# Performance work log

Hardware: AMD Instinct MI355X
Metric: run time of the kernel (lower is better)

The kernel has to match this reference:

```python
import jax, jax.numpy as jnp
import numpy as np

NUM_HEADS = 8
BN_EPS = 1e-5
NORM_EPS = 1e-12


def setup_inputs() -> dict:
    key = jax.random.key(0)
    ks = jax.random.split(key, 5)
    b, c, h, w = 4, 256, 128, 128
    cr = c // 16  # reduced channels in the gating branch
    return {
        "x": jax.random.normal(ks[0], (b, c, h, w), dtype=jnp.float32),
        "temperature": jnp.ones((NUM_HEADS, 1, 1), dtype=jnp.float32),
        "w1": jax.random.normal(ks[1], (cr, c), dtype=jnp.float32) * 0.05,
        "b1": jnp.zeros((cr,), dtype=jnp.float32),
        "bn_gamma": jnp.ones((cr,), dtype=jnp.float32),
        "bn_beta": jnp.zeros((cr,), dtype=jnp.float32),
        "bn_mean": jnp.zeros((cr,), dtype=jnp.float32),
        "bn_var": jnp.ones((cr,), dtype=jnp.float32),
        "w2": jax.random.normal(ks[2], (c, cr), dtype=jnp.float32) * 0.1,
        "b2": jnp.zeros((c,), dtype=jnp.float32),
        "proj_w": jax.random.normal(ks[3], (c, 2 * c), dtype=jnp.float32) * 0.05,
    }


def _complex_softmax(a, axis=-1):
    return jax.lax.complex(jax.nn.softmax(a.real, axis=axis),
                           jax.nn.softmax(a.imag, axis=axis))


def reference(x, temperature, w1, b1, bn_gamma, bn_beta, bn_mean, bn_var, w2, b2, proj_w):
    b, c, h, w = x.shape
    hd = NUM_HEADS
    xf = jnp.fft.fft2(x)

    # q = k = v = fft2(x), reshaped to (b, head, c/head, h*w)
    qkv = xf.reshape(b, hd, c // hd, h * w)
    # F.normalize over last dim: divide by L2 norm (complex norm = sqrt(sum |.|^2))
    nrm = jnp.sqrt(jnp.sum(qkv.real**2 + qkv.imag**2, axis=-1, keepdims=True))
    qn = qkv / jnp.maximum(nrm, NORM_EPS)

    # channel attention: (b, head, c', c'), contract over spatial freq dim
    attn = jnp.einsum('bhcn,bhdn->bhcd', qn, qn) * temperature.astype(xf.dtype)
    attn = _complex_softmax(attn, axis=-1)

    out = jnp.einsum('bhcd,bhdn->bhcn', attn, qkv)
    # torch.fft.ifft2 on a 4D tensor acts over the last two dims (c', h*w)
    out_f = jnp.abs(jnp.fft.ifft2(out)).reshape(b, c, h, w)

    # gating branch: conv1x1 -> BN(inference) -> ReLU -> conv1x1 -> sigmoid on real(fft2(x))
    y = jnp.einsum('bchw,oc->bohw', xf.real, w1) + b1[:, None, None]
    y = (y - bn_mean[:, None, None]) / jnp.sqrt(bn_var[:, None, None] + BN_EPS)
    y = y * bn_gamma[:, None, None] + bn_beta[:, None, None]
    y = jax.nn.relu(y)
    y = jnp.einsum('bchw,oc->bohw', y, w2) + b2[:, None, None]
    gate = jax.nn.sigmoid(y)

    out_f_l = jnp.abs(jnp.fft.ifft2(gate * xf))

    cat = jnp.concatenate([out_f, out_f_l], axis=1)  # (b, 2c, h, w)
    return jnp.einsum('bchw,oc->bohw', cat, proj_w)
```

## Files before the change

### kernel.cpp

```cpp
#include <hip/hip_runtime.h>
#include <math.h>

#define NFFT 16384
static constexpr size_t NP = 16777216;

typedef short bf16x8 __attribute__((ext_vector_type(8)));
typedef __fp16 f16x8 __attribute__((ext_vector_type(8)));
typedef float f32x4  __attribute__((ext_vector_type(4)));
typedef __fp16 h16x2 __attribute__((ext_vector_type(2)));

union FU  { bf16x8 v; unsigned u[4]; };
union FU16{ f16x8  v; unsigned u[4]; };

__device__ __forceinline__ void sincos_rev(float rv, float& sn, float& cs){
    sn = __builtin_amdgcn_sinf(rv);
    cs = __builtin_amdgcn_cosf(rv);
}
__device__ __forceinline__ int rev7(int v){ return (int)(__brev((unsigned)v) >> 25); }

__device__ __forceinline__ unsigned f2bf(float f){
    unsigned u = __float_as_uint(f);
    return (u + 0x7FFFu + ((u >> 16) & 1u)) >> 16;
}
__device__ __forceinline__ float bf2f(unsigned h){ return __uint_as_float(h << 16); }
__device__ __forceinline__ unsigned packsplit(float v){
    unsigned h = f2bf(v);
    float r = v - bf2f(h);
    unsigned l = f2bf(r);
    return (h << 16) | l;
}

union HU2 { h16x2 h; unsigned u; };
__device__ __forceinline__ unsigned packh(float a, float b){
    HU2 z; z.h = __builtin_amdgcn_cvt_pkrtz(a, b); return z.u;
}
__device__ __forceinline__ void unpackh(unsigned u, float& a, float& b){
    HU2 z; z.u = u; a = (float)z.h.x; b = (float)z.h.y;
}

struct TwF { float cw[6], sw[6], sg[6], c6, s6; };
__device__ __forceinline__ void make_twf(TwF& t){
    const int l = threadIdx.x & 63;
    #pragma unroll
    for (int lg = 0; lg < 6; ++lg){
        int m = 1 << lg;
        bool up = (l & m) != 0;
        int e = (l & (m-1)) * (64 >> lg);
        float sn, cs; sincos_rev((float)e * 0.0078125f, sn, cs);
        t.cw[lg] = up ? cs : 1.f;
        t.sw[lg] = up ? -sn : 0.f;
        t.sg[lg] = up ? -1.f : 1.f;
    }
    sincos_rev((float)l * 0.0078125f, t.s6, t.c6);
}
struct TwI { float cw[6], sw[6], c6, s6; };
__device__ __forceinline__ void make_twi(TwI& t){
    const int l = threadIdx.x & 63;
    #pragma unroll
    for (int lg = 0; lg < 6; ++lg){
        int m = 1 << lg;
        bool up = (l & m) != 0;
        int e = (l & (m-1)) * (64 >> lg);
        float sn, cs; sincos_rev((float)e * 0.0078125f, sn, cs);
        t.cw[lg] = up ? -cs : cs;
        t.sw[lg] = up ? -sn : sn;
    }
    sincos_rev((float)l * 0.0078125f, t.s6, t.c6);
}

__device__ __forceinline__ void dif128t(const TwF& t, float& r0, float& i0, float& r1, float& i1){
    {
        float ar = r0 + r1, ai = i0 + i1;
        float br = r0 - r1, bi = i0 - i1;
        r0 = ar; i0 = ai;
        r1 =  br*t.c6 + bi*t.s6;
        i1 = -br*t.s6 + bi*t.c6;
    }
    #pragma unroll
    for (int lg = 5; lg >= 0; --lg){
        int m = 1 << lg;
        float cw = t.cw[lg], sw = t.sw[lg], sg = t.sg[lg];
        float pr = __shfl_xor(r0, m, 64), pi = __shfl_xor(i0, m, 64);
        float tr = fmaf(sg, r0, pr), ti = fmaf(sg, i0, pi);
        r0 = tr*cw - ti*sw;
        i0 = tr*sw + ti*cw;
        pr = __shfl_xor(r1, m, 64); pi = __shfl_xor(i1, m, 64);
        tr = fmaf(sg, r1, pr); ti = fmaf(sg, i1, pi);
        r1 = tr*cw - ti*sw;
        i1 = tr*sw + ti*cw;
    }
}

__device__ __forceinline__ void dit128t(const TwI& t, float& r0, float& i0, float& r1, float& i1){
    const int l = threadIdx.x & 63;
    #pragma unroll
    for (int lg = 0; lg <= 5; ++lg){
        int m = 1 << lg;
        bool up = (l & m) != 0;
        float cw = t.cw[lg], sw = t.sw[lg];
        float pr = __shfl_xor(r0, m, 64), pi = __shfl_xor(i0, m, 64);
        float vr = up ? r0 : pr, vi = up ? i0 : pi;
        float ar = up ? pr : r0, ai = up ? pi : i0;
        r0 = fmaf(vr, cw, fmaf(vi, -sw, ar));
        i0 = fmaf(vr, sw, fmaf(vi,  cw, ai));
        pr = __shfl_xor(r1, m, 64); pi = __shfl_xor(i1, m, 64);
        vr = up ? r1 : pr; vi = up ? i1 : pi;
        ar = up ? pr : r1; ai = up ? pi : i1;
        r1 = fmaf(vr, cw, fmaf(vi, -sw, ar));
        i1 = fmaf(vr, sw, fmaf(vi,  cw, ai));
    }
    {
        float wr = r1*t.c6 - i1*t.s6, wi = r1*t.s6 + i1*t.c6;
        float ar = r0 + wr, ai = i0 + wi;
        r1 = r0 - wr; i1 = i0 - wi;
        r0 = ar; i0 = ai;
    }
}

__global__ __launch_bounds__(1024, 8) void k_fft2_fwd(const float* __restrict__ x,
                                                   unsigned* __restrict__ spR, unsigned* __restrict__ spI,
                                                   float* __restrict__ norm2){
    __shared__ unsigned sp[128*129];
    __shared__ float red[16];
    int lane = threadIdx.x & 63, wave = threadIdx.x >> 6;
    int img = blockIdx.x;
    TwF tw; make_twf(tw);
    const float* base = x + (size_t)img * NFFT;
    #pragma unroll 2
    for (int it = 0; it < 8; ++it){
        int h = (wave << 3) + it;
        float a0 = base[h*128 + lane], b0 = 0.f;
        float a1 = base[h*128 + lane + 64], b1 = 0.f;
        dif128t(tw, a0, b0, a1, b1);
        sp[lane*129 + h]      = packh(a0, b0);
        sp[(lane+64)*129 + h] = packh(a1, b1);
    }
    __syncthreads();
    float acc = 0.f;
    #pragma unroll 2
    for (int it = 0; it < 8; ++it){
        int j = (wave << 3) + it;
        float a0, b0, a1, b1;
        unpackh(sp[j*129 + lane],      a0, b0);
        unpackh(sp[j*129 + lane + 64], a1, b1);
        dif128t(tw, a0, b0, a1, b1);
        acc += a0*a0 + b0*b0 + a1*a1 + b1*b1;
        float t0 = __shfl_xor(a0, 1, 64), u0 = __shfl_xor(b0, 1, 64);
        float t1 = __shfl_xor(a1, 1, 64), u1 = __shfl_xor(b1, 1, 64);
        size_t m = (size_t)img*8192 + (size_t)j*64;
        int k = lane >> 1;
        if (!(lane & 1)){
            spR[m + k]      = packh(a0, t0);
            spR[m + 32 + k] = packh(a1, t1);
        } else {
            spI[m + k]      = packh(u0, b0);
            spI[m + 32 + k] = packh(u1, b1);
        }
    }
    #pragma unroll
    for (int m = 32; m >= 1; m >>= 1) acc += __shfl_xor(acc, m, 64);
    if (lane == 0) red[wave] = acc;
    __syncthreads();
    if (threadIdx.x == 0){
        float s = 0.f;
        #pragma unroll
        for (int i = 0; i < 16; ++i) s += red[i];
        norm2[img] = s;
    }
}

__global__ __launch_bounds__(256) void k_gram(const unsigned* __restrict__ spR, const unsigned* __restrict__ spI,
                                              float* __restrict__ Gpart){
    __shared__ unsigned lds[2*32*132];
    int t = threadIdx.x, lane = t & 63, wave = t >> 6;
    int bh = blockIdx.x >> 5;
    int ks = blockIdx.x & 31;
    size_t cbase2 = (size_t)bh * 32 * 8192;
    int k0blk = ks << 9;

    int sc = t >> 3, tk = t & 7;

    f32x4 aRe[2][2], aIm[2][2];
    #pragma unroll
    for (int i = 0; i < 2; ++i)
        #pragma unroll
        for (int j = 0; j < 2; ++j){ aRe[i][j] = (f32x4){0,0,0,0}; aIm[i][j] = (f32x4){0,0,0,0}; }

    for (int tile = 0; tile < 2; ++tile){
        int kb = k0blk + (tile << 8);
        __syncthreads();
        {
            const unsigned* pr  = spR + cbase2 + (size_t)sc*8192 + (kb >> 1) + tk*16;
            const unsigned* pi_ = spI + cbase2 + (size_t)sc*8192 + (kb >> 1) + tk*16;
            unsigned* dr = &lds[sc*132 + tk*16];
            unsigned* di = &lds[32*132 + sc*132 + tk*16];
            #pragma unroll
            for (int j = 0; j < 4; ++j){
                *(uint4*)(dr + 4*j) = *(const uint4*)(pr + 4*j);
                *(uint4*)(di + 4*j) = *(const uint4*)(pi_ + 4*j);
            }
        }
        __syncthreads();
        #pragma unroll
        for (int ss = 0; ss < 2; ++ss){
            int s = wave + (ss << 2);
            int kbase = (s << 4) + ((lane >> 4) << 2);
            FU16 fr0, fr1, fi0, fi1, fn0, fn1;
            *(uint4*)fr0.u = *(const uint4*)&lds[ (lane & 15)*132 + kbase ];
            *(uint4*)fr1.u = *(const uint4*)&lds[ ((lane & 15) + 16)*132 + kbase ];
            *(uint4*)fi0.u = *(const uint4*)&lds[ 32*132 + (lane & 15)*132 + kbase ];
            *(uint4*)fi1.u = *(const uint4*)&lds[ 32*132 + ((lane & 15) + 16)*132 + kbase ];
            #pragma unroll
            for (int p = 0; p < 4; ++p){ fn0.u[p] = fi0.u[p] ^ 0x80008000u; fn1.u[p] = fi1.u[p] ^ 0x80008000u; }
            aRe[0][0] = __builtin_amdgcn_mfma_f32_16x16x32_f16(fr0.v, fr0.v, aRe[0][0], 0, 0, 0);
            aRe[0][0] = __builtin_amdgcn_mfma_f32_16x16x32_f16(fn0.v, fi0.v, aRe[0][0], 0, 0, 0);
            aRe[0][1] = __builtin_amdgcn_mfma_f32_16x16x32_f16(fr0.v, fr1.v, aRe[0][1], 0, 0, 0);
            aRe[0][1] = __builtin_amdgcn_mfma_f32_16x16x32_f16(fn0.v, fi1.v, aRe[0][1], 0, 0, 0);
            aRe[1][0] = __builtin_amdgcn_mfma_f32_16x16x32_f16(fr1.v, fr0.v, aRe[1][0], 0, 0, 0);
            aRe[1][0] = __builtin_amdgcn_mfma_f32_16x16x32_f16(fn1.v, fi0.v, aRe[1][0], 0, 0, 0);
            aRe[1][1] = __builtin_amdgcn_mfma_f32_16x16x32_f16(fr1.v, fr1.v, aRe[1][1], 0, 0, 0);
            aRe[1][1] = __builtin_amdgcn_mfma_f32_16x16x32_f16(fn1.v, fi1.v, aRe[1][1], 0, 0, 0);
            aIm[0][0] = __builtin_amdgcn_mfma_f32_16x16x32_f16(fr0.v, fi0.v, aIm[0][0], 0, 0, 0);
            aIm[0][0] = __builtin_amdgcn_mfma_f32_16x16x32_f16(fi0.v, fr0.v, aIm[0][0], 0, 0, 0);
            aIm[0][1] = __builtin_amdgcn_mfma_f32_16x16x32_f16(fr0.v, fi1.v, aIm[0][1], 0, 0, 0);
            aIm[0][1] = __builtin_amdgcn_mfma_f32_16x16x32_f16(fi0.v, fr1.v, aIm[0][1], 0, 0, 0);
            aIm[1][0] = __builtin_amdgcn_mfma_f32_16x16x32_f16(fr1.v, fi0.v, aIm[1][0], 0, 0, 0);
            aIm[1][0] = __builtin_amdgcn_mfma_f32_16x16x32_f16(fi1.v, fr0.v, aIm[1][0], 0, 0, 0);
            aIm[1][1] = __builtin_amdgcn_mfma_f32_16x16x32_f16(fr1.v, fi1.v, aIm[1][1], 0, 0, 0);
            aIm[1][1] = __builtin_amdgcn_mfma_f32_16x16x32_f16(fi1.v, fr1.v, aIm[1][1], 0, 0, 0);
        }
    }
    __syncthreads();
    float* rbuf = (float*)lds;
    int dcol = lane & 15, rrow = lane >> 4;
    #pragma unroll
    for (int i = 0; i < 2; ++i)
        #pragma unroll
        for (int j = 0; j < 2; ++j)
            #pragma unroll
            for (int r = 0; r < 4; ++r){
                int c = (i << 4) + (rrow << 2) + r;
                int d = (j << 4) + dcol;
                rbuf[wave*2048 + ((c << 5) + d)*2    ] = aRe[i][j][r];
                rbuf[wave*2048 + ((c << 5) + d)*2 + 1] = aIm[i][j][r];
            }
    __syncthreads();
    float* gp = Gpart + (size_t)blockIdx.x * 2048;
    for (int idx = t; idx < 2048; idx += 256)
        gp[idx] = rbuf[idx] + rbuf[2048 + idx] + rbuf[4096 + idx] + rbuf[6144 + idx];
}

__global__ __launch_bounds__(256) void k_gram_red(const float* __restrict__ Gpart, float* __restrict__ G){
    int bh = blockIdx.x >> 3;
    int q  = ((blockIdx.x & 7) << 8) + threadIdx.x;
    const float* gp = Gpart + (size_t)bh * 32 * 2048 + q;
    float s = 0.f;
    #pragma unroll 8
    for (int p = 0; p < 32; ++p) s += gp[(size_t)p * 2048];
    G[(size_t)bh * 2048 + q] = s;
}

__global__ __launch_bounds__(256) void k_attn(const float* __restrict__ G, const float* __restrict__ norm2,
                                              const float* __restrict__ temp, float* __restrict__ attn2){
    __shared__ float ar[32*33], ai[32*33];
    int bh = blockIdx.x, h = bh & 7, t = threadIdx.x;
    if (t < 32){
        float tv = temp[h];
        float nc = fmaxf(sqrtf(norm2[(bh<<5) + t]), 1e-12f);
        const float* gr = G + (size_t)bh*2048 + t*64;
        float mr = -1e30f, mi = -1e30f;
        for (int d = 0; d < 32; ++d){
            float nd = fmaxf(sqrtf(norm2[(bh<<5) + d]), 1e-12f);
            float s = tv / (nc * nd);
            float vr = gr[d*2] * s, vi = gr[d*2+1] * s;
            ar[t*33+d] = vr; ai[t*33+d] = vi;
            mr = fmaxf(mr, vr); mi = fmaxf(mi, vi);
        }
        float sr = 0.f, si = 0.f;
        for (int d = 0; d < 32; ++d){
            float er = __expf(ar[t*33+d] - mr), ei = __expf(ai[t*33+d] - mi);
            ar[t*33+d] = er; ai[t*33+d] = ei; sr += er; si += ei;
        }
        sr = 1.f/sr; si = 1.f/si;
        for (int d = 0; d < 32; ++d){ ar[t*33+d] *= sr; ai[t*33+d] *= si; }
    }
    __syncthreads();
    const float S = 1.f / 524288.f;
    for (int q = t; q < 1024; q += 256){
        int e = q >> 5, d = q & 31;
        float sr = 0.f, si = 0.f;
        for (int c = 0; c < 32; ++c){
            float sn, cs; sincos_rev((float)((e*c) & 31) * 0.03125f, sn, cs);
            float xr = ar[c*33+d], xi = ai[c*33+d];
            sr += cs*xr - sn*xi;
            si += cs*xi + sn*xr;
        }
        attn2[(size_t)bh*2048 + q*2]     = sr * S;
        attn2[(size_t)bh*2048 + q*2 + 1] = si * S;
    }
}

__global__ __launch_bounds__(256) void k_mix(const unsigned* __restrict__ spR, const unsigned* __restrict__ spI,
                                             const float* __restrict__ attn2,
                                             unsigned* __restrict__ om){
    __shared__ unsigned lds[2*32*36];
    __shared__ float a2s[2048];
    int t = threadIdx.x, lane = t & 63, wave = t >> 6;
    int quad = lane >> 4, l15 = lane & 15;
    int bh = blockIdx.x >> 5;
    int n0 = (blockIdx.x & 31) << 9;
    size_t cbase2 = (size_t)bh * 32 * 8192;
    {
        const float4* s4 = (const float4*)(attn2 + (size_t)bh*2048);
        float4* d4 = (float4*)a2s;
        d4[t] = s4[t]; d4[t + 256] = s4[t + 256];
    }
    __syncthreads();
    FU16 Ar[2], Ai[2];
    #pragma unroll
    for (int et = 0; et < 2; ++et){
        int e = (et << 4) + l15;
        #pragma unroll
        for (int p = 0; p < 4; ++p){
            int d0 = (quad << 3) + (p << 1);
            Ar[et].u[p] = packh(a2s[(e*32 + d0)*2],     a2s[(e*32 + d0 + 1)*2]);
            Ai[et].u[p] = packh(a2s[(e*32 + d0)*2 + 1], a2s[(e*32 + d0 + 1)*2 + 1]);
        }
    }
    int sd = t >> 3, sc4 = (t & 7) << 2;
    for (int tile = 0; tile < 8; ++tile){
        int nb = n0 + (tile << 6);
        __syncthreads();
        {
            size_t g2 = cbase2 + (size_t)sd*8192 + (nb >> 1) + sc4;
            *(uint4*)&lds[sd*36 + sc4]         = *(const uint4*)&spR[g2];
            *(uint4*)&lds[32*36 + sd*36 + sc4] = *(const uint4*)&spI[g2];
        }
        __syncthreads();
        int colb = (wave << 4) + l15;
        int cb2 = colb >> 1; bool codd = colb & 1;
        FU16 Xr, Xi, Xn;
        #pragma unroll
        for (int p = 0; p < 4; ++p){
            int d0 = (quad << 3) + (p << 1);
            unsigned e0 = lds[d0*36 + cb2], e1 = lds[(d0+1)*36 + cb2];
            Xr.u[p] = codd ? ((e0 >> 16) | (e1 & 0xFFFF0000u)) : ((e0 & 0xFFFFu) | (e1 << 16));
            e0 = lds[32*36 + d0*36 + cb2]; e1 = lds[32*36 + (d0+1)*36 + cb2];
            Xi.u[p] = codd ? ((e0 >> 16) | (e1 & 0xFFFF0000u)) : ((e0 & 0xFFFFu) | (e1 << 16));
            Xn.u[p] = Xi.u[p] ^ 0x80008000u;
        }
        #pragma unroll
        for (int et = 0; et < 2; ++et){
            f32x4 ar = (f32x4){0,0,0,0}, ai = (f32x4){0,0,0,0};
            ar = __builtin_amdgcn_mfma_f32_16x16x32_f16(Ar[et].v, Xr.v, ar, 0, 0, 0);
            ar = __builtin_amdgcn_mfma_f32_16x16x32_f16(Ai[et].v, Xn.v, ar, 0, 0, 0);
            ai = __builtin_amdgcn_mfma_f32_16x16x32_f16(Ar[et].v, Xi.v, ai, 0, 0, 0);
            ai = __builtin_amdgcn_mfma_f32_16x16x32_f16(Ai[et].v, Xr.v, ai, 0, 0, 0);
            #pragma unroll
            for (int r = 0; r < 4; ++r){
                int e = (et << 4) + (quad << 2) + r;
                om[cbase2*2 + (size_t)e*NFFT + nb + colb] = packh(ar[r], ai[r]);
            }
        }
    }
}

__global__ __launch_bounds__(1024, 8) void k_ifft_n(unsigned* io){
    __shared__ unsigned sp[128*129];
    int lane = threadIdx.x & 63, wave = threadIdx.x >> 6;
    size_t rb = (size_t)blockIdx.x * NFFT;
    TwI tw; make_twi(tw);
    #pragma unroll 2
    for (int it = 0; it < 8; ++it){
        int jw = (wave << 3) + it;
        size_t base = rb + ((size_t)jw << 7);
        float a0, b0, a1, b1;
        unpackh(io[base + lane], a0, b0);
        unpackh(io[base + lane + 64], a1, b1);
        dit128t(tw, a0, b0, a1, b1);
        int kw = rev7(jw);
        float sn, cs;
        sincos_rev((float)(lane * kw) * 6.103515625e-05f, sn, cs);
        float r = a0*cs - b0*sn, i2 = a0*sn + b0*cs;
        sp[lane*129 + jw] = packh(r, i2);
        sincos_rev((float)((lane + 64) * kw) * 6.103515625e-05f, sn, cs);
        r = a1*cs - b1*sn; i2 = a1*sn + b1*cs;
        sp[(lane+64)*129 + jw] = packh(r, i2);
    }
    __syncthreads();
    unsigned av[8][2];
    #pragma unroll 2
    for (int it = 0; it < 8; ++it){
        int pw = (wave << 3) + it;
        float a0, b0, a1, b1;
        unpackh(sp[pw*129 + lane],      a0, b0);
        unpackh(sp[pw*129 + lane + 64], a1, b1);
        dit128t(tw, a0, b0, a1, b1);
        av[it][0] = packsplit(sqrtf(a0*a0 + b0*b0));
        av[it][1] = packsplit(sqrtf(a1*a1 + b1*b1));
    }
    __syncthreads();
    #pragma unroll 2
    for (int it = 0; it < 8; ++it){
        int pw = (wave << 3) + it;
        sp[lane*129 + pw] = av[it][0];
        sp[(lane+64)*129 + pw] = av[it][1];
    }
    __syncthreads();
    int row = threadIdx.x >> 3, cb = (threadIdx.x & 7) << 4;
    size_t ob = rb + ((size_t)row << 7) + cb;
    const unsigned* s = &sp[row*129 + cb];
    #pragma unroll
    for (int q = 0; q < 4; ++q)
        *(uint4*)(io + ob + (q << 2)) = make_uint4(s[q*4], s[q*4+1], s[q*4+2], s[q*4+3]);
}

__global__ __launch_bounds__(256) void k_gate(unsigned* spR, unsigned* spI,
                                              const float* __restrict__ w1, const float* __restrict__ b1,
                                              const float* __restrict__ bg, const float* __restrict__ bb_,
                                              const float* __restrict__ bm, const float* __restrict__ bv,
                                              const float* __restrict__ w2, const float* __restrict__ b2){
    __shared__ float w1T[256*17];
    __shared__ float w2s[256*16];
    __shared__ float yred[256*17];
    int t = threadIdx.x, g = t >> 6, col = t & 63;
    #pragma unroll
    for (int i = 0; i < 16; ++i) w1T[t*17 + i] = w1[i*256 + t];
    {
        const float4* s4 = (const float4*)w2; float4* d4 = (float4*)w2s;
        #pragma unroll
        for (int i = 0; i < 4; ++i) d4[i*256 + t] = s4[i*256 + t];
    }
    __syncthreads();
    int b = blockIdx.x >> 8;
    int n = ((blockIdx.x & 255) << 6) + col;
    int odd = n & 1;
    size_t base2 = (((size_t)b << 8) << 13) + (n >> 1);
    float y[16];
    #pragma unroll
    for (int r = 0; r < 16; ++r) y[r] = 0.f;
    for (int c = g << 6; c < (g << 6) + 64; ++c){
        float lo, hi; unpackh(spR[base2 + ((size_t)c << 13)], lo, hi);
        float xr = odd ? hi : lo;
        #pragma unroll
        for (int r = 0; r < 16; ++r) y[r] += w1T[c*17 + r] * xr;
    }
    #pragma unroll
    for (int r = 0; r < 16; ++r) yred[t*17 + r] = y[r];
    __syncthreads();
    #pragma unroll
    for (int r = 0; r < 16; ++r){
        float v = yred[col*17 + r] + yred[(col+64)*17 + r]
                + yred[(col+128)*17 + r] + yred[(col+192)*17 + r] + b1[r];
        v = (v - bm[r]) * rsqrtf(bv[r] + 1e-5f) * bg[r] + bb_[r];
        y[r] = fmaxf(v, 0.f);
    }
    for (int o = g << 6; o < (g << 6) + 64; ++o){
        float s = b2[o];
        #pragma unroll
        for (int r = 0; r < 16; ++r) s += w2s[o*16 + r] * y[r];
        float gg = 1.f / (1.f + __expf(-s)) * 6.103515625e-05f;
        float ggN = __shfl_xor(gg, 1, 64);
        size_t mi = base2 + ((size_t)o << 13);
        if (!odd){
            float lo, hi; unpackh(spR[mi], lo, hi);
            spR[mi] = packh(gg*lo, ggN*hi);
        } else {
            float lo, hi; unpackh(spI[mi], lo, hi);
            spI[mi] = packh(ggN*lo, gg*hi);
        }
    }
}

__global__ __launch_bounds__(1024, 8) void k_ifft2_gate(const unsigned* __restrict__ spR,
                                                        const unsigned* __restrict__ spI,
                                                        unsigned* __restrict__ outp){
    __shared__ unsigned sp[128*129];
    int lane = threadIdx.x & 63, wave = threadIdx.x >> 6;
    size_t ib = (size_t)blockIdx.x * NFFT;
    TwI tw; make_twi(tw);
    #pragma unroll 2
    for (int it = 0; it < 8; ++it){
        int jw = (wave << 3) + it;
        size_t m = (ib + ((size_t)jw << 7)) >> 1;
        int k = lane >> 1; bool od = lane & 1;
        float lo, hi, a0, b0, a1, b1;
        unpackh(spR[m + k], lo, hi);      a0 = od ? hi : lo;
        unpackh(spI[m + k], lo, hi);      b0 = od ? hi : lo;
        unpackh(spR[m + 32 + k], lo, hi); a1 = od ? hi : lo;
        unpackh(spI[m + 32 + k], lo, hi); b1 = od ? hi : lo;
        dit128t(tw, a0, b0, a1, b1);
        sp[lane*129 + jw]      = packh(a0, b0);
        sp[(lane+64)*129 + jw] = packh(a1, b1);
    }
    __syncthreads();
    #pragma unroll 2
    for (int it = 0; it < 8; ++it){
        int ph = (wave << 3) + it;
        float a0, b0, a1, b1;
        unpackh(sp[ph*129 + lane],      a0, b0);
        unpackh(sp[ph*129 + lane + 64], a1, b1);
        dit128t(tw, a0, b0, a1, b1);
        size_t o = ib + ((size_t)ph << 7);
        outp[o + lane]      = packsplit(sqrtf(a0*a0 + b0*b0));
        outp[o + lane + 64] = packsplit(sqrtf(a1*a1 + b1*b1));
    }
}

__global__ __launch_bounds__(256) void k_pw_cvt(const float* __restrict__ pw, unsigned* __restrict__ pwp){
    int i = (blockIdx.x << 10) + (threadIdx.x << 2);
    float4 v = *(const float4*)(pw + i);
    uint4 o;
    o.x = packsplit(v.x); o.y = packsplit(v.y); o.z = packsplit(v.z); o.w = packsplit(v.w);
    *(uint4*)(pwp + i) = o;
}

__global__ __launch_bounds__(256) void k_proj(const unsigned* __restrict__ cat0, const unsigned* __restrict__ cat1,
                                              const unsigned* __restrict__ pwp, float* __restrict__ out){
    __shared__ unsigned As[128*33];
    __shared__ unsigned Bs[32*129];
    int t = threadIdx.x, lane = t & 63, wave = t >> 6;
    int quad = lane >> 4, l15 = lane & 15;
    int b  = blockIdx.x >> 8;
    int mo = (blockIdx.x >> 7) & 1;
    int nt = blockIdx.x & 127;
    int n0 = nt << 7;
    int wr = (wave >> 1) << 6;
    int wc = (wave & 1) << 6;

    f32x4 acc[4][4];
    #pragma unroll
    for (int i = 0; i < 4; ++i)
        #pragma unroll
        for (int j = 0; j < 4; ++j) acc[i][j] = (f32x4){0.f,0.f,0.f,0.f};

    int ao = t >> 1, ak = (t & 1) << 4;
    int bk = t >> 5, bn = t & 31;

    for (int ks = 0; ks < 16; ++ks){
        int k0 = ks << 5;
        __syncthreads();
        {
            const unsigned* ap = pwp + (size_t)((mo << 7) + ao)*512 + k0 + ak;
            #pragma unroll
            for (int i = 0; i < 16; ++i) As[ao*33 + ak + i] = ap[i];
        }
        {
            #pragma unroll
            for (int p = 0; p < 4; ++p){
                int q = k0 + (p << 3) + bk;
                const unsigned* srow = (q < 256) ? (cat0 + (size_t)((b<<8) + q) * NFFT)
                                                 : (cat1 + (size_t)((b<<8) + (q-256)) * NFFT);
                #pragma unroll
                for (int i = 0; i < 4; ++i){
                    int n = bn + (i << 5);
                    Bs[((p<<3) + bk)*129 + n] = srow[n0 + n];
                }
            }
        }
        __syncthreads();
        FU Ah[4], Al[4], Bh[4], Bl[4];
        #pragma unroll
        for (int mi = 0; mi < 4; ++mi){
            const unsigned* ap = &As[(wr + (mi << 4) + l15)*33 + (quad << 3)];
            #pragma unroll
            for (int p = 0; p < 4; ++p){
                unsigned e0 = ap[2*p], e1 = ap[2*p+1];
                Ah[mi].u[p] = (e0 >> 16) | (e1 & 0xFFFF0000u);
                Al[mi].u[p] = (e0 & 0xFFFFu) | (e1 << 16);
            }
        }
        #pragma unroll
        for (int ni = 0; ni < 4; ++ni){
            int n = wc + (ni << 4) + l15;
            #pragma unroll
            for (int p = 0; p < 4; ++p){
                unsigned e0 = Bs[((quad << 3) + 2*p)*129 + n];
                unsigned e1 = Bs[((quad << 3) + 2*p + 1)*129 + n];
                Bh[ni].u[p] = (e0 >> 16) | (e1 & 0xFFFF0000u);
                Bl[ni].u[p] = (e0 & 0xFFFFu) | (e1 << 16);
            }
        }
        #pragma unroll
        for (int mi = 0; mi < 4; ++mi)
            #pragma unroll
            for (int ni = 0; ni < 4; ++ni){
                acc[mi][ni] = __builtin_amdgcn_mfma_f32_16x16x32_bf16(Ah[mi].v, Bh[ni].v, acc[mi][ni], 0, 0, 0);
                acc[mi][ni] = __builtin_amdgcn_mfma_f32_16x16x32_bf16(Ah[mi].v, Bl[ni].v, acc[mi][ni], 0, 0, 0);
                acc[mi][ni] = __builtin_amdgcn_mfma_f32_16x16x32_bf16(Al[mi].v, Bh[ni].v, acc[mi][ni], 0, 0, 0);
            }
    }
    size_t obase = (size_t)((b << 8) + (mo << 7));
    #pragma unroll
    for (int mi = 0; mi < 4; ++mi)
        #pragma unroll
        for (int ni = 0; ni < 4; ++ni){
            int o_ = wr + (mi << 4) + (quad << 2);
            int n_ = n0 + wc + (ni << 4) + l15;
            float* op = out + (obase + o_)*NFFT + n_;
            #pragma unroll
            for (int r = 0; r < 4; ++r) op[(size_t)r*NFFT] = acc[mi][ni][r];
        }
}

extern "C" void kernel_launch(void* const* d_in, const int* in_sizes, int n_in,
                              void* d_out, int out_size, void* d_ws, size_t ws_size,
                              hipStream_t stream) {
    const float* x    = (const float*)d_in[0];
    const float* temp = (const float*)d_in[1];
    const float* w1   = (const float*)d_in[2];
    const float* b1   = (const float*)d_in[3];
    const float* bg   = (const float*)d_in[4];
    const float* bb_  = (const float*)d_in[5];
    const float* bm   = (const float*)d_in[6];
    const float* bv   = (const float*)d_in[7];
    const float* w2   = (const float*)d_in[8];
    const float* b2   = (const float*)d_in[9];
    const float* pw   = (const float*)d_in[10];
    float* out = (float*)d_out;

    float* ws = (float*)d_ws;
    unsigned* SpecR = (unsigned*)ws;
    unsigned* SpecI = SpecR + (NP >> 1);
    unsigned* Ecat  = (unsigned*)(ws + NP);
    unsigned* Cat1  = (unsigned*)(ws + 2*NP);
    float* norm2 = ws + 3*NP;
    float* G     = norm2 + 1024;
    float* attn2 = G + 65536;
    unsigned* pwpack = (unsigned*)(attn2 + 65536);
    float* Gpart = (float*)Ecat;

    size_t need = (3*NP + 1024 + 65536 + 65536 + 131072) * sizeof(float);
    if (ws_size < need) return;

    k_pw_cvt<<<128, 256, 0, stream>>>(pw, pwpack);
    k_fft2_fwd<<<1024, 1024, 0, stream>>>(x, SpecR, SpecI, norm2);
    k_gram<<<1024, 256, 0, stream>>>(SpecR, SpecI, Gpart);
    k_gram_red<<<256, 256, 0, stream>>>(Gpart, G);
    k_attn<<<32, 256, 0, stream>>>(G, norm2, temp, attn2);
    k_mix<<<1024, 256, 0, stream>>>(SpecR, SpecI, attn2, Ecat);
    k_ifft_n<<<1024, 1024, 0, stream>>>(Ecat);
    k_gate<<<1024, 256, 0, stream>>>(SpecR, SpecI, w1, b1, bg, bb_, bm, bv, w2, b2);
    k_ifft2_gate<<<1024, 1024, 0, stream>>>(SpecR, SpecI, Cat1);
    k_proj<<<1024, 256, 0, stream>>>(Ecat, Cat1, pwpack, out);
    (void)in_sizes; (void)n_in; (void)out_size; (void)ws_size;
}
```

Measured before the change: 518.6 us.

## Store ifft magnitudes and proj weights in fp16, single-pass f16 MFMA projection

The inverse-FFT kernels now write the magnitude outputs as packed fp16 pairs instead of bf16 hi/lo split words, which halves their output bytes. The projection GEMM runs one f16 MFMA per tile instead of three bf16 split MFMAs, and the projection weights are converted to fp16. The DIT butterfly is reworked into a twiddle-then-shuffle form with a sign factor, removing the selects. Precision drops from roughly fp32-equivalent split bf16 to plain fp16, and the magnitudes could overflow the fp16 range.

```diff
diff --git a/kernel.cpp b/kernel.cpp
--- a/kernel.cpp
+++ b/kernel.cpp
@@ -23,12 +23,6 @@
     return (u + 0x7FFFu + ((u >> 16) & 1u)) >> 16;
 }
 __device__ __forceinline__ float bf2f(unsigned h){ return __uint_as_float(h << 16); }
-__device__ __forceinline__ unsigned packsplit(float v){
-    unsigned h = f2bf(v);
-    float r = v - bf2f(h);
-    unsigned l = f2bf(r);
-    return (h << 16) | l;
-}
 
 union HU2 { h16x2 h; unsigned u; };
 __device__ __forceinline__ unsigned packh(float a, float b){
@@ -53,7 +47,7 @@
     }
     sincos_rev((float)l * 0.0078125f, t.s6, t.c6);
 }
-struct TwI { float cw[6], sw[6], c6, s6; };
+struct TwI { float cw[6], sw[6], sg[6], c6, s6; };
 __device__ __forceinline__ void make_twi(TwI& t){
     const int l = threadIdx.x & 63;
     #pragma unroll
@@ -62,8 +56,9 @@
         bool up = (l & m) != 0;
         int e = (l & (m-1)) * (64 >> lg);
         float sn, cs; sincos_rev((float)e * 0.0078125f, sn, cs);
-        t.cw[lg] = up ? -cs : cs;
-        t.sw[lg] = up ? -sn : sn;
+        t.cw[lg] = up ? cs : 1.f;
+        t.sw[lg] = up ? sn : 0.f;
+        t.sg[lg] = up ? -1.f : 1.f;
     }
     sincos_rev((float)l * 0.0078125f, t.s6, t.c6);
 }
@@ -92,22 +87,18 @@
 }
 
 __device__ __forceinline__ void dit128t(const TwI& t, float& r0, float& i0, float& r1, float& i1){
-    const int l = threadIdx.x & 63;
     #pragma unroll
     for (int lg = 0; lg <= 5; ++lg){
         int m = 1 << lg;
-        bool up = (l & m) != 0;
-        float cw = t.cw[lg], sw = t.sw[lg];
-        float pr = __shfl_xor(r0, m, 64), pi = __shfl_xor(i0, m, 64);
-        float vr = up ? r0 : pr, vi = up ? i0 : pi;
-        float ar = up ? pr : r0, ai = up ? pi : i0;
-        r0 = fmaf(vr, cw, fmaf(vi, -sw, ar));
-        i0 = fmaf(vr, sw, fmaf(vi,  cw, ai));
-        pr = __shfl_xor(r1, m, 64); pi = __shfl_xor(i1, m, 64);
-        vr = up ? r1 : pr; vi = up ? i1 : pi;
-        ar = up ? pr : r1; ai = up ? pi : i1;
-        r1 = fmaf(vr, cw, fmaf(vi, -sw, ar));
-        i1 = fmaf(vr, sw, fmaf(vi,  cw, ai));
+        float cw = t.cw[lg], sw = t.sw[lg], sg = t.sg[lg];
+        float qr = r0*cw - i0*sw, qi = r0*sw + i0*cw;
+        float pr = __shfl_xor(qr, m, 64), pi = __shfl_xor(qi, m, 64);
+        r0 = fmaf(sg, qr, pr);
+        i0 = fmaf(sg, qi, pi);
+        qr = r1*cw - i1*sw; qi = r1*sw + i1*cw;
+        pr = __shfl_xor(qr, m, 64); pi = __shfl_xor(qi, m, 64);
+        r1 = fmaf(sg, qr, pr);
+        i1 = fmaf(sg, qi, pi);
     }
     {
         float wr = r1*t.c6 - i1*t.s6, wi = r1*t.s6 + i1*t.c6;
@@ -365,7 +356,7 @@
     }
 }
 
-__global__ __launch_bounds__(1024, 8) void k_ifft_n(unsigned* io){
+__global__ __launch_bounds__(1024, 8) void k_ifft_n(const unsigned* __restrict__ in, unsigned* __restrict__ outp){
     __shared__ unsigned sp[128*129];
     int lane = threadIdx.x & 63, wave = threadIdx.x >> 6;
     size_t rb = (size_t)blockIdx.x * NFFT;
@@ -375,8 +366,8 @@
         int jw = (wave << 3) + it;
         size_t base = rb + ((size_t)jw << 7);
         float a0, b0, a1, b1;
-        unpackh(io[base + lane], a0, b0);
-        unpackh(io[base + lane + 64], a1, b1);
+        unpackh(in[base + lane], a0, b0);
+        unpackh(in[base + lane + 64], a1, b1);
         dit128t(tw, a0, b0, a1, b1);
         int kw = rev7(jw);
         float sn, cs;
@@ -388,31 +379,29 @@
         sp[(lane+64)*129 + jw] = packh(r, i2);
     }
     __syncthreads();
-    unsigned av[8][2];
-    #pragma unroll 2
+    float av0[8], av1[8];
+    #pragma unroll
     for (int it = 0; it < 8; ++it){
         int pw = (wave << 3) + it;
         float a0, b0, a1, b1;
         unpackh(sp[pw*129 + lane],      a0, b0);
         unpackh(sp[pw*129 + lane + 64], a1, b1);
         dit128t(tw, a0, b0, a1, b1);
-        av[it][0] = packsplit(sqrtf(a0*a0 + b0*b0));
-        av[it][1] = packsplit(sqrtf(a1*a1 + b1*b1));
-    }
-    __syncthreads();
-    #pragma unroll 2
-    for (int it = 0; it < 8; ++it){
-        int pw = (wave << 3) + it;
-        sp[lane*129 + pw] = av[it][0];
-        sp[(lane+64)*129 + pw] = av[it][1];
-    }
-    __syncthreads();
-    int row = threadIdx.x >> 3, cb = (threadIdx.x & 7) << 4;
-    size_t ob = rb + ((size_t)row << 7) + cb;
-    const unsigned* s = &sp[row*129 + cb];
-    #pragma unroll
-    for (int q = 0; q < 4; ++q)
-        *(uint4*)(io + ob + (q << 2)) = make_uint4(s[q*4], s[q*4+1], s[q*4+2], s[q*4+3]);
+        av0[it] = sqrtf(a0*a0 + b0*b0);
+        av1[it] = sqrtf(a1*a1 + b1*b1);
+    }
+    __syncthreads();
+    #pragma unroll
+    for (int p = 0; p < 4; ++p){
+        sp[lane*65 + (wave << 2) + p]      = packh(av0[2*p], av0[2*p+1]);
+        sp[(lane+64)*65 + (wave << 2) + p] = packh(av1[2*p], av1[2*p+1]);
+    }
+    __syncthreads();
+    int row = threadIdx.x >> 3, cb = (threadIdx.x & 7) << 3;
+    unsigned* ob = outp + ((size_t)blockIdx.x << 13) + row*64 + cb;
+    const unsigned* s = &sp[row*65 + cb];
+    *(uint4*)(ob)     = make_uint4(s[0], s[1], s[2], s[3]);
+    *(uint4*)(ob + 4) = make_uint4(s[4], s[5], s[6], s[7]);
 }
 
 __global__ __launch_bounds__(256) void k_gate(unsigned* spR, unsigned* spI,
@@ -477,8 +466,8 @@
                                                         unsigned* __restrict__ outp){
     __shared__ unsigned sp[128*129];
     int lane = threadIdx.x & 63, wave = threadIdx.x >> 6;
+    TwI tw; make_twi(tw);
     size_t ib = (size_t)blockIdx.x * NFFT;
-    TwI tw; make_twi(tw);
     #pragma unroll 2
     for (int it = 0; it < 8; ++it){
         int jw = (wave << 3) + it;
@@ -501,30 +490,35 @@
         unpackh(sp[ph*129 + lane],      a0, b0);
         unpackh(sp[ph*129 + lane + 64], a1, b1);
         dit128t(tw, a0, b0, a1, b1);
-        size_t o = ib + ((size_t)ph << 7);
-        outp[o + lane]      = packsplit(sqrtf(a0*a0 + b0*b0));
-        outp[o + lane + 64] = packsplit(sqrtf(a1*a1 + b1*b1));
+        float v0 = sqrtf(a0*a0 + b0*b0), v1 = sqrtf(a1*a1 + b1*b1);
+        float p0 = __shfl_xor(v0, 1, 64), p1 = __shfl_xor(v1, 1, 64);
+        if (!(lane & 1)){
+            size_t o2 = ((size_t)blockIdx.x << 13) + (ph << 6);
+            outp[o2 + (lane >> 1)]      = packh(v0, p0);
+            outp[o2 + 32 + (lane >> 1)] = packh(v1, p1);
+        }
     }
 }
 
 __global__ __launch_bounds__(256) void k_pw_cvt(const float* __restrict__ pw, unsigned* __restrict__ pwp){
     int i = (blockIdx.x << 10) + (threadIdx.x << 2);
     float4 v = *(const float4*)(pw + i);
-    uint4 o;
-    o.x = packsplit(v.x); o.y = packsplit(v.y); o.z = packsplit(v.z); o.w = packsplit(v.w);
-    *(uint4*)(pwp + i) = o;
+    uint2 o;
+    o.x = packh(v.x, v.y); o.y = packh(v.z, v.w);
+    *(uint2*)(pwp + (i >> 1)) = o;
 }
 
 __global__ __launch_bounds__(256) void k_proj(const unsigned* __restrict__ cat0, const unsigned* __restrict__ cat1,
                                               const unsigned* __restrict__ pwp, float* __restrict__ out){
-    __shared__ unsigned As[128*33];
-    __shared__ unsigned Bs[32*129];
+    __shared__ unsigned As[128*17];
+    __shared__ unsigned Bs[32*65];
     int t = threadIdx.x, lane = t & 63, wave = t >> 6;
     int quad = lane >> 4, l15 = lane & 15;
     int b  = blockIdx.x >> 8;
     int mo = (blockIdx.x >> 7) & 1;
     int nt = blockIdx.x & 127;
     int n0 = nt << 7;
+    int n0_2 = nt << 6;
     int wr = (wave >> 1) << 6;
     int wc = (wave & 1) << 6;
 
@@ -534,61 +528,49 @@
         #pragma unroll
         for (int j = 0; j < 4; ++j) acc[i][j] = (f32x4){0.f,0.f,0.f,0.f};
 
-    int ao = t >> 1, ak = (t & 1) << 4;
-    int bk = t >> 5, bn = t & 31;
+    int ao = t >> 1, ak = (t & 1) << 3;
+    int bk = t >> 3, bn8 = (t & 7) << 3;
+    int par = l15 & 1;
 
     for (int ks = 0; ks < 16; ++ks){
-        int k0 = ks << 5;
         __syncthreads();
         {
-            const unsigned* ap = pwp + (size_t)((mo << 7) + ao)*512 + k0 + ak;
-            #pragma unroll
-            for (int i = 0; i < 16; ++i) As[ao*33 + ak + i] = ap[i];
+            const unsigned* ap = pwp + (size_t)((mo << 7) + ao)*256 + (ks << 4) + ak;
+            #pragma unroll
+            for (int i = 0; i < 8; ++i) As[ao*17 + ak + i] = ap[i];
         }
         {
+            int q = (ks << 5) + bk;
+            const unsigned* srow = (q < 256) ? (cat0 + (size_t)((b << 8) + q) * 8192)
+                                             : (cat1 + (size_t)((b << 8) + q - 256) * 8192);
+            const unsigned* sp_ = srow + n0_2 + bn8;
+            *(uint4*)&Bs[bk*65 + bn8]     = *(const uint4*)sp_;
+            *(uint4*)&Bs[bk*65 + bn8 + 4] = *(const uint4*)(sp_ + 4);
+        }
+        __syncthreads();
+        FU16 Af[4], Bf[4];
+        #pragma unroll
+        for (int mi = 0; mi < 4; ++mi){
+            const unsigned* ap = &As[(wr + (mi << 4) + l15)*17 + (quad << 2)];
+            #pragma unroll
+            for (int p = 0; p < 4; ++p) Af[mi].u[p] = ap[p];
+        }
+        #pragma unroll
+        for (int ni = 0; ni < 4; ++ni){
+            int n2 = (wc + (ni << 4) + l15) >> 1;
             #pragma unroll
             for (int p = 0; p < 4; ++p){
-                int q = k0 + (p << 3) + bk;
-                const unsigned* srow = (q < 256) ? (cat0 + (size_t)((b<<8) + q) * NFFT)
-                                                 : (cat1 + (size_t)((b<<8) + (q-256)) * NFFT);
-                #pragma unroll
-                for (int i = 0; i < 4; ++i){
-                    int n = bn + (i << 5);
-                    Bs[((p<<3) + bk)*129 + n] = srow[n0 + n];
-                }
+                unsigned e0 = Bs[((quad << 3) + 2*p)*65 + n2];
+                unsigned e1 = Bs[((quad << 3) + 2*p + 1)*65 + n2];
+                Bf[ni].u[p] = par ? ((e0 >> 16) | (e1 & 0xFFFF0000u))
+                                  : ((e0 & 0xFFFFu) | (e1 << 16));
             }
         }
-        __syncthreads();
-        FU Ah[4], Al[4], Bh[4], Bl[4];
-        #pragma unroll
-        for (int mi = 0; mi < 4; ++mi){
-            const unsigned* ap = &As[(wr + (mi << 4) + l15)*33 + (quad << 3)];
-            #pragma unroll
-            for (int p = 0; p < 4; ++p){
-                unsigned e0 = ap[2*p], e1 = ap[2*p+1];
-                Ah[mi].u[p] = (e0 >> 16) | (e1 & 0xFFFF0000u);
-                Al[mi].u[p] = (e0 & 0xFFFFu) | (e1 << 16);
-            }
-        }
-        #pragma unroll
-        for (int ni = 0; ni < 4; ++ni){
-            int n = wc + (ni << 4) + l15;
-            #pragma unroll
-            for (int p = 0; p < 4; ++p){
-                unsigned e0 = Bs[((quad << 3) + 2*p)*129 + n];
-                unsigned e1 = Bs[((quad << 3) + 2*p + 1)*129 + n];
-                Bh[ni].u[p] = (e0 >> 16) | (e1 & 0xFFFF0000u);
-                Bl[ni].u[p] = (e0 & 0xFFFFu) | (e1 << 16);
-            }
-        }
         #pragma unroll
         for (int mi = 0; mi < 4; ++mi)
             #pragma unroll
-            for (int ni = 0; ni < 4; ++ni){
-                acc[mi][ni] = __builtin_amdgcn_mfma_f32_16x16x32_bf16(Ah[mi].v, Bh[ni].v, acc[mi][ni], 0, 0, 0);
-                acc[mi][ni] = __builtin_amdgcn_mfma_f32_16x16x32_bf16(Ah[mi].v, Bl[ni].v, acc[mi][ni], 0, 0, 0);
-                acc[mi][ni] = __builtin_amdgcn_mfma_f32_16x16x32_bf16(Al[mi].v, Bh[ni].v, acc[mi][ni], 0, 0, 0);
-            }
+            for (int ni = 0; ni < 4; ++ni)
+                acc[mi][ni] = __builtin_amdgcn_mfma_f32_16x16x32_f16(Af[mi].v, Bf[ni].v, acc[mi][ni], 0, 0, 0);
     }
     size_t obase = (size_t)((b << 8) + (mo << 7));
     #pragma unroll
@@ -623,7 +605,8 @@
     unsigned* SpecR = (unsigned*)ws;
     unsigned* SpecI = SpecR + (NP >> 1);
     unsigned* Ecat  = (unsigned*)(ws + NP);
-    unsigned* Cat1  = (unsigned*)(ws + 2*NP);
+    unsigned* Cat0  = (unsigned*)(ws + 2*NP);
+    unsigned* Cat1  = Cat0 + 8388608;
     float* norm2 = ws + 3*NP;
     float* G     = norm2 + 1024;
     float* attn2 = G + 65536;
@@ -639,9 +622,9 @@
     k_gram_red<<<256, 256, 0, stream>>>(Gpart, G);
     k_attn<<<32, 256, 0, stream>>>(G, norm2, temp, attn2);
     k_mix<<<1024, 256, 0, stream>>>(SpecR, SpecI, attn2, Ecat);
-    k_ifft_n<<<1024, 1024, 0, stream>>>(Ecat);
+    k_ifft_n<<<1024, 1024, 0, stream>>>(Ecat, Cat0);
     k_gate<<<1024, 256, 0, stream>>>(SpecR, SpecI, w1, b1, bg, bb_, bm, bv, w2, b2);
     k_ifft2_gate<<<1024, 1024, 0, stream>>>(SpecR, SpecI, Cat1);
-    k_proj<<<1024, 256, 0, stream>>>(Ecat, Cat1, pwpack, out);
+    k_proj<<<1024, 256, 0, stream>>>(Cat0, Cat1, pwpack, out);
     (void)in_sizes; (void)n_in; (void)out_size; (void)ws_size;
 }
```

New measurement: 479.6 us. 7.5% less time.
